# Kernel optimization log

Measured on AMD Instinct MI355X. Metric: run time of the kernel, lower is better.

The kernel has to match this reference:

```python
import jax, jax.numpy as jnp
import numpy as np

N = 16      # manifold_dim
H = 128     # hidden_dim
B = 256     # batch
EPS = 1e-6


def setup_inputs() -> dict:
    key = jax.random.key(0)
    ks = jax.random.split(key, 14)
    def w(k, shape):
        fan_in = shape[0]
        return jax.random.uniform(k, shape, jnp.float32, -1.0, 1.0) / np.sqrt(fan_in)
    return {
        "points": jax.random.normal(ks[0], (B, N), jnp.float32),
        # metric network: N -> H -> N*N
        "mW1": w(ks[1], (N, H)), "mb1": jnp.zeros((H,), jnp.float32),
        "mW2": w(ks[2], (H, N * N)), "mb2": jnp.zeros((N * N,), jnp.float32),
        # christoffel network: 3 -> H -> 1
        "cW1": w(ks[3], (3, H)), "cb1": jnp.zeros((H,), jnp.float32),
        "cW2": w(ks[4], (H, 1)), "cb2": jnp.zeros((1,), jnp.float32),
        # ricci network: 4N -> 2H -> N*N
        "rW1": w(ks[5], (4 * N, 2 * H)), "rb1": jnp.zeros((2 * H,), jnp.float32),
        "rW2": w(ks[6], (2 * H, N * N)), "rb2": jnp.zeros((N * N,), jnp.float32),
    }


def reference(points, mW1, mb1, mW2, mb2, cW1, cb1, cW2, cb2, rW1, rb1, rW2, rb2):
    b = points.shape[0]
    n = N
    # ---- metric: (b, n, n) ----
    mh = jax.nn.relu(points @ mW1 + mb1)
    metric = (mh @ mW2 + mb2).reshape(b, n, n)
    metric = metric + EPS * jnp.eye(n, dtype=metric.dtype)
    metric = 0.5 * (metric + jnp.swapaxes(metric, -2, -1))

    # ---- christoffel: vectorized over all (i,j,k) triples ----
    # inputs per triple: [metric_ij, metric_jk, metric_ki]
    m_ij = jnp.broadcast_to(metric[:, :, :, None], (b, n, n, n))
    m_jk = jnp.broadcast_to(metric[:, None, :, :], (b, n, n, n))
    mT = jnp.swapaxes(metric, -2, -1)  # mT[b,i,k] = metric[b,k,i]
    m_ki = jnp.broadcast_to(mT[:, :, None, :], (b, n, n, n))
    ch_in = jnp.stack([m_ij, m_jk, m_ki], axis=-1)        # (b,n,n,n,3)
    ch_h = jnp.tanh(ch_in @ cW1 + cb1)                    # (b,n,n,n,H)
    christoffel = (ch_h @ cW2 + cb2)[..., 0]              # (b,n,n,n)

    # ---- ricci: vectorized over all (i,j) pairs ----
    p_b = jnp.broadcast_to(points[:, None, None, :], (b, n, n, n))
    m_i = jnp.broadcast_to(metric[:, :, None, :], (b, n, n, n))
    m_j = jnp.broadcast_to(metric[:, None, :, :], (b, n, n, n))
    r_in = jnp.concatenate([p_b, m_i, m_j, christoffel], axis=-1)  # (b,n,n,4n)
    r_h = jax.nn.relu(r_in @ rW1 + rb1)                   # (b,n,n,2H)
    r_out = (r_h @ rW2 + rb2).reshape(b, n, n, n, n)      # (b,i,j,n,n)
    r_out = 0.5 * (r_out + jnp.swapaxes(r_out, -1, -2))
    ricci = r_out.sum(axis=(1, 2)) / (n * n)              # (b,n,n)
    return ricci
```

## Files before the change

kernel.cpp:

```cpp
#include <hip/hip_runtime.h>
#include <hip/hip_bf16.h>

#define NDIM 16
#define HDIM 128
#define BATCH 256
#define EPS_D 1e-6f

typedef float v2f __attribute__((ext_vector_type(2)));
static __device__ __forceinline__ v2f v2(float a, float b) {
  v2f r; r.x = a; r.y = b; return r;
}
static __device__ __forceinline__ v2f splat(float a) {
  v2f r; r.x = a; r.y = a; return r;
}

__global__ __launch_bounds__(256) void metric_proj_kernel(
    const float* __restrict__ points,
    const float* __restrict__ mW1, const float* __restrict__ mb1,
    const float* __restrict__ mW2, const float* __restrict__ mb2,
    const float* __restrict__ rW1, const float* __restrict__ rb1,
    float* __restrict__ metric,
    float* __restrict__ A1, float* __restrict__ Mi, float* __restrict__ Mj,
    float* __restrict__ G) {
  int b = blockIdx.x;
  int t = threadIdx.x;
  __shared__ float p[16];
  __shared__ float mh[128];
  __shared__ float raw[256];
  __shared__ float M[256];
  G[b * 256 + t] = 0.f;
  if (t < 16) p[t] = points[b * 16 + t];
  __syncthreads();
  if (t < 128) {
    float acc = mb1[t];
#pragma unroll
    for (int k = 0; k < 16; ++k) acc = fmaf(p[k], mW1[k * 128 + t], acc);
    mh[t] = fmaxf(acc, 0.f);
  }
  __syncthreads();
  {
    float acc = mb2[t];
#pragma unroll 8
    for (int h = 0; h < 128; ++h) acc = fmaf(mh[h], mW2[h * 256 + t], acc);
    raw[t] = acc;
  }
  __syncthreads();
  {
    int i = t >> 4, j = t & 15;
    float v = 0.5f * (raw[i * 16 + j] + raw[j * 16 + i]);
    if (i == j) v += EPS_D;
    M[t] = v;
    metric[b * 256 + t] = v;
  }
  __syncthreads();
  {
    int h = t;
    float wB[16], wC[16];
#pragma unroll
    for (int c = 0; c < 16; ++c) {
      wB[c] = rW1[(16 + c) * 256 + h];
      wC[c] = rW1[(32 + c) * 256 + h];
    }
    float a = rb1[h];
#pragma unroll
    for (int r = 0; r < 16; ++r) a = fmaf(p[r], rW1[r * 256 + h], a);
    A1[b * 256 + h] = a;
#pragma unroll 2
    for (int i = 0; i < 16; ++i) {
      float mi = 0.f, mj = 0.f;
#pragma unroll
      for (int c = 0; c < 16; ++c) {
        float m = M[i * 16 + c];
        mi = fmaf(m, wB[c], mi);
        mj = fmaf(m, wC[c], mj);
      }
      Mi[(b * 16 + i) * 256 + h] = mi;
      Mj[(b * 16 + i) * 256 + h] = mj;
    }
  }
}

__global__ __launch_bounds__(128, 8) void chr_kernel(
    const float* __restrict__ metric,
    const float* __restrict__ cW1, const float* __restrict__ cb1,
    const float* __restrict__ cW2, const float* __restrict__ cb2,
    const float* __restrict__ rW1,
    const float* __restrict__ A1, const float* __restrict__ Mi,
    const float* __restrict__ Mj,
    float* __restrict__ G) {
  int bi = blockIdx.x;
  int b = bi >> 4, i = bi & 15;
  int t = threadIdx.x;
  int w = t >> 6, l = t & 63;
  __shared__ float M[256];
  __shared__ float4 z[128];
  __shared__ float4 w2p[32];
  __shared__ float4 ch4[64];
  float* chf = (float*)ch4;
  M[t] = metric[b * 256 + t];
  M[t + 128] = metric[b * 256 + t + 128];
  {
    const float S = 2.8853900817779268f;
    z[t] = make_float4(S * cW1[t], S * cW1[128 + t], S * cW1[256 + t],
                       S * cb1[t]);
    ((float*)w2p)[t] = cW2[t];
  }
  __syncthreads();

  {
    int jk0 = w * 128 + l, jk1 = jk0 + 64;
    int j0 = jk0 >> 4, k0 = jk0 & 15;
    int j1 = jk1 >> 4, k1 = jk1 & 15;
    v2f x0 = v2(M[i * 16 + j0], M[i * 16 + j1]);
    v2f x1 = v2(M[j0 * 16 + k0], M[j1 * 16 + k1]);
    v2f x2 = v2(M[k0 * 16 + i], M[k1 * 16 + i]);
    v2f acc = splat(cb2[0]);
    for (int hq = 0; hq < 32; ++hq) {
      float4 W2 = w2p[hq];
      float w2u[4] = {W2.x, W2.y, W2.z, W2.w};
#pragma unroll
      for (int u = 0; u < 4; ++u) {
        float4 Q = z[hq * 4 + u];
        v2f pre = __builtin_elementwise_fma(
            x0, splat(Q.x),
            __builtin_elementwise_fma(
                x1, splat(Q.y),
                __builtin_elementwise_fma(x2, splat(Q.z), splat(Q.w))));
        v2f e;
        e.x = __builtin_amdgcn_exp2f(pre.x);
        e.y = __builtin_amdgcn_exp2f(pre.y);
        v2f ep = e + splat(1.f);
        v2f r;
        r.x = __builtin_amdgcn_rcpf(ep.x);
        r.y = __builtin_amdgcn_rcpf(ep.y);
        v2f th = __builtin_elementwise_fma(splat(-2.f), r, splat(1.f));
        acc = __builtin_elementwise_fma(th, splat(w2u[u]), acc);
      }
    }
    chf[jk0] = acc.x;
    chf[jk1] = acc.y;
  }
  __syncthreads();

  {
    int h2 = 2 * t;
    v2f rc2[16];
#pragma unroll
    for (int kk = 0; kk < 16; ++kk) {
      float2 rv = *(const float2*)&rW1[(48 + kk) * 256 + h2];
      rc2[kk] = v2(rv.x, rv.y);
    }
    float2 a1v = *(const float2*)&A1[b * 256 + h2];
    float2 miv = *(const float2*)&Mi[bi * 256 + h2];
    v2f base = v2(a1v.x + miv.x, a1v.y + miv.y);
    v2f hacc = splat(0.f);
    for (int jj = 0; jj < 16; ++jj) {
      float4 c0 = ch4[jj * 4 + 0];
      float4 c1 = ch4[jj * 4 + 1];
      float4 c2v = ch4[jj * 4 + 2];
      float4 c3 = ch4[jj * 4 + 3];
      float2 mjv = *(const float2*)&Mj[(b * 16 + jj) * 256 + h2];
      v2f cp = base + v2(mjv.x, mjv.y);
      float cc[16] = {c0.x, c0.y, c0.z, c0.w, c1.x, c1.y, c1.z, c1.w,
                      c2v.x, c2v.y, c2v.z, c2v.w, c3.x, c3.y, c3.z, c3.w};
#pragma unroll
      for (int kk = 0; kk < 16; ++kk)
        cp = __builtin_elementwise_fma(splat(cc[kk]), rc2[kk], cp);
      v2f rl;
      rl.x = fmaxf(cp.x, 0.f);
      rl.y = fmaxf(cp.y, 0.f);
      hacc += rl;
    }
    atomicAdd(&G[b * 256 + h2], hacc.x);
    atomicAdd(&G[b * 256 + h2 + 1], hacc.y);
  }
}

__global__ __launch_bounds__(256) void final_kernel(
    const float* __restrict__ G,
    const float* __restrict__ rW2, const float* __restrict__ rb2,
    float* __restrict__ out) {
  int b = blockIdx.x;
  int t = threadIdx.x;
  __shared__ float4 Gs[64];
  __shared__ float T[256];
  if (t < 64) Gs[t] = ((const float4*)(G + b * 256))[t];
  __syncthreads();
  float acc = 256.f * rb2[t];
#pragma unroll 4
  for (int h4 = 0; h4 < 64; ++h4) {
    float4 gg = Gs[h4];
    acc = fmaf(gg.x, rW2[(h4 * 4 + 0) * 256 + t], acc);
    acc = fmaf(gg.y, rW2[(h4 * 4 + 1) * 256 + t], acc);
    acc = fmaf(gg.z, rW2[(h4 * 4 + 2) * 256 + t], acc);
    acc = fmaf(gg.w, rW2[(h4 * 4 + 3) * 256 + t], acc);
  }
  T[t] = acc * (1.f / 256.f);
  __syncthreads();
  int k = t >> 4, lcol = t & 15;
  out[b * 256 + t] = 0.5f * (T[k * 16 + lcol] + T[lcol * 16 + k]);
}

extern "C" void kernel_launch(void* const* d_in, const int* in_sizes, int n_in,
                              void* d_out, int out_size, void* d_ws, size_t ws_size,
                              hipStream_t stream) {
  const float* points = (const float*)d_in[0];
  const float* mW1 = (const float*)d_in[1];
  const float* mb1 = (const float*)d_in[2];
  const float* mW2 = (const float*)d_in[3];
  const float* mb2 = (const float*)d_in[4];
  const float* cW1 = (const float*)d_in[5];
  const float* cb1 = (const float*)d_in[6];
  const float* cW2 = (const float*)d_in[7];
  const float* cb2 = (const float*)d_in[8];
  const float* rW1 = (const float*)d_in[9];
  const float* rb1 = (const float*)d_in[10];
  const float* rW2 = (const float*)d_in[11];
  const float* rb2 = (const float*)d_in[12];
  float* out = (float*)d_out;

  float* ws = (float*)d_ws;
  float* metric = ws;
  float* A1 = metric + 65536;
  float* Mi = A1 + 65536;
  float* Mj = Mi + 1048576;
  float* G = Mj + 1048576;

  metric_proj_kernel<<<BATCH, 256, 0, stream>>>(points, mW1, mb1, mW2, mb2,
                                                rW1, rb1, metric, A1, Mi, Mj, G);
  chr_kernel<<<BATCH * NDIM, 128, 0, stream>>>(metric, cW1, cb1, cW2, cb2, rW1,
                                               A1, Mi, Mj, G);
  final_kernel<<<BATCH, 256, 0, stream>>>(G, rW2, rb2, out);
}
```

Measured before the change: 134.0 us.

## Process two i-rows per chr_kernel block to reuse loaded weights and halve atomics

Each chr_kernel block now handles two i values instead of one: each wave computes the Christoffel values for a full i row (four outputs per lane), and the ricci stage reuses the rW1 register tile and the Mj loads for both rows. This halves the grid, the per-block setup (loading M, z and w2p), the rW1 and Mj reloads, and the atomicAdds into G. In exchange it raises register pressure (launch bounds relaxed from 8 to 4 blocks per CU) and cuts the number of blocks, which could lower occupancy and latency hiding.

```diff
diff --git a/kernel.cpp b/kernel.cpp
--- a/kernel.cpp
+++ b/kernel.cpp
@@ -80,7 +80,7 @@
   }
 }
 
-__global__ __launch_bounds__(128, 8) void chr_kernel(
+__global__ __launch_bounds__(128, 4) void chr_kernel(
     const float* __restrict__ metric,
     const float* __restrict__ cW1, const float* __restrict__ cb1,
     const float* __restrict__ cW2, const float* __restrict__ cb2,
@@ -88,15 +88,15 @@
     const float* __restrict__ A1, const float* __restrict__ Mi,
     const float* __restrict__ Mj,
     float* __restrict__ G) {
-  int bi = blockIdx.x;
-  int b = bi >> 4, i = bi & 15;
+  int blk = blockIdx.x;
+  int b = blk >> 3, ip = blk & 7;
   int t = threadIdx.x;
   int w = t >> 6, l = t & 63;
+  int i = ip * 2 + w;
   __shared__ float M[256];
   __shared__ float4 z[128];
   __shared__ float4 w2p[32];
-  __shared__ float4 ch4[64];
-  float* chf = (float*)ch4;
+  __shared__ float4 ch4[2][64];
   M[t] = metric[b * 256 + t];
   M[t + 128] = metric[b * 256 + t + 128];
   {
@@ -108,42 +108,63 @@
   __syncthreads();
 
   {
-    int jk0 = w * 128 + l, jk1 = jk0 + 64;
-    int j0 = jk0 >> 4, k0 = jk0 & 15;
-    int j1 = jk1 >> 4, k1 = jk1 & 15;
-    v2f x0 = v2(M[i * 16 + j0], M[i * 16 + j1]);
-    v2f x1 = v2(M[j0 * 16 + k0], M[j1 * 16 + k1]);
-    v2f x2 = v2(M[k0 * 16 + i], M[k1 * 16 + i]);
-    v2f acc = splat(cb2[0]);
+    float* chf = (float*)ch4[w];
+    int jA0 = l >> 4, kA0 = l & 15;
+    int jA1 = (l + 64) >> 4, kA1 = (l + 64) & 15;
+    int jB0 = (l + 128) >> 4, kB0 = (l + 128) & 15;
+    int jB1 = (l + 192) >> 4, kB1 = (l + 192) & 15;
+    v2f x0A = v2(M[i * 16 + jA0], M[i * 16 + jA1]);
+    v2f x1A = v2(M[jA0 * 16 + kA0], M[jA1 * 16 + kA1]);
+    v2f x2A = v2(M[kA0 * 16 + i], M[kA1 * 16 + i]);
+    v2f x0B = v2(M[i * 16 + jB0], M[i * 16 + jB1]);
+    v2f x1B = v2(M[jB0 * 16 + kB0], M[jB1 * 16 + kB1]);
+    v2f x2B = v2(M[kB0 * 16 + i], M[kB1 * 16 + i]);
+    v2f accA = splat(cb2[0]);
+    v2f accB = splat(cb2[0]);
     for (int hq = 0; hq < 32; ++hq) {
       float4 W2 = w2p[hq];
       float w2u[4] = {W2.x, W2.y, W2.z, W2.w};
 #pragma unroll
       for (int u = 0; u < 4; ++u) {
         float4 Q = z[hq * 4 + u];
-        v2f pre = __builtin_elementwise_fma(
-            x0, splat(Q.x),
+        v2f preA = __builtin_elementwise_fma(
+            x0A, splat(Q.x),
             __builtin_elementwise_fma(
-                x1, splat(Q.y),
-                __builtin_elementwise_fma(x2, splat(Q.z), splat(Q.w))));
-        v2f e;
-        e.x = __builtin_amdgcn_exp2f(pre.x);
-        e.y = __builtin_amdgcn_exp2f(pre.y);
-        v2f ep = e + splat(1.f);
-        v2f r;
-        r.x = __builtin_amdgcn_rcpf(ep.x);
-        r.y = __builtin_amdgcn_rcpf(ep.y);
-        v2f th = __builtin_elementwise_fma(splat(-2.f), r, splat(1.f));
-        acc = __builtin_elementwise_fma(th, splat(w2u[u]), acc);
+                x1A, splat(Q.y),
+                __builtin_elementwise_fma(x2A, splat(Q.z), splat(Q.w))));
+        v2f preB = __builtin_elementwise_fma(
+            x0B, splat(Q.x),
+            __builtin_elementwise_fma(
+                x1B, splat(Q.y),
+                __builtin_elementwise_fma(x2B, splat(Q.z), splat(Q.w))));
+        v2f eA, eB;
+        eA.x = __builtin_amdgcn_exp2f(preA.x);
+        eA.y = __builtin_amdgcn_exp2f(preA.y);
+        eB.x = __builtin_amdgcn_exp2f(preB.x);
+        eB.y = __builtin_amdgcn_exp2f(preB.y);
+        v2f epA = eA + splat(1.f);
+        v2f epB = eB + splat(1.f);
+        v2f rA, rB;
+        rA.x = __builtin_amdgcn_rcpf(epA.x);
+        rA.y = __builtin_amdgcn_rcpf(epA.y);
+        rB.x = __builtin_amdgcn_rcpf(epB.x);
+        rB.y = __builtin_amdgcn_rcpf(epB.y);
+        v2f thA = __builtin_elementwise_fma(splat(-2.f), rA, splat(1.f));
+        v2f thB = __builtin_elementwise_fma(splat(-2.f), rB, splat(1.f));
+        accA = __builtin_elementwise_fma(thA, splat(w2u[u]), accA);
+        accB = __builtin_elementwise_fma(thB, splat(w2u[u]), accB);
       }
     }
-    chf[jk0] = acc.x;
-    chf[jk1] = acc.y;
+    chf[l] = accA.x;
+    chf[l + 64] = accA.y;
+    chf[l + 128] = accB.x;
+    chf[l + 192] = accB.y;
   }
   __syncthreads();
 
   {
     int h2 = 2 * t;
+    int bi0 = b * 16 + ip * 2, bi1 = bi0 + 1;
     v2f rc2[16];
 #pragma unroll
     for (int kk = 0; kk < 16; ++kk) {
@@ -151,28 +172,44 @@
       rc2[kk] = v2(rv.x, rv.y);
     }
     float2 a1v = *(const float2*)&A1[b * 256 + h2];
-    float2 miv = *(const float2*)&Mi[bi * 256 + h2];
-    v2f base = v2(a1v.x + miv.x, a1v.y + miv.y);
-    v2f hacc = splat(0.f);
+    float2 mi0 = *(const float2*)&Mi[bi0 * 256 + h2];
+    float2 mi1 = *(const float2*)&Mi[bi1 * 256 + h2];
+    v2f base0 = v2(a1v.x + mi0.x, a1v.y + mi0.y);
+    v2f base1 = v2(a1v.x + mi1.x, a1v.y + mi1.y);
+    v2f hacc0 = splat(0.f);
+    v2f hacc1 = splat(0.f);
     for (int jj = 0; jj < 16; ++jj) {
-      float4 c0 = ch4[jj * 4 + 0];
-      float4 c1 = ch4[jj * 4 + 1];
-      float4 c2v = ch4[jj * 4 + 2];
-      float4 c3 = ch4[jj * 4 + 3];
       float2 mjv = *(const float2*)&Mj[(b * 16 + jj) * 256 + h2];
-      v2f cp = base + v2(mjv.x, mjv.y);
-      float cc[16] = {c0.x, c0.y, c0.z, c0.w, c1.x, c1.y, c1.z, c1.w,
-                      c2v.x, c2v.y, c2v.z, c2v.w, c3.x, c3.y, c3.z, c3.w};
-#pragma unroll
-      for (int kk = 0; kk < 16; ++kk)
-        cp = __builtin_elementwise_fma(splat(cc[kk]), rc2[kk], cp);
-      v2f rl;
-      rl.x = fmaxf(cp.x, 0.f);
-      rl.y = fmaxf(cp.y, 0.f);
-      hacc += rl;
-    }
-    atomicAdd(&G[b * 256 + h2], hacc.x);
-    atomicAdd(&G[b * 256 + h2 + 1], hacc.y);
+      v2f mj2 = v2(mjv.x, mjv.y);
+      float4 c0 = ch4[0][jj * 4 + 0];
+      float4 c1 = ch4[0][jj * 4 + 1];
+      float4 c2v = ch4[0][jj * 4 + 2];
+      float4 c3 = ch4[0][jj * 4 + 3];
+      float4 d0 = ch4[1][jj * 4 + 0];
+      float4 d1 = ch4[1][jj * 4 + 1];
+      float4 d2v = ch4[1][jj * 4 + 2];
+      float4 d3 = ch4[1][jj * 4 + 3];
+      v2f cp0 = base0 + mj2;
+      v2f cp1 = base1 + mj2;
+      float cc0[16] = {c0.x, c0.y, c0.z, c0.w, c1.x, c1.y, c1.z, c1.w,
+                       c2v.x, c2v.y, c2v.z, c2v.w, c3.x, c3.y, c3.z, c3.w};
+      float cc1[16] = {d0.x, d0.y, d0.z, d0.w, d1.x, d1.y, d1.z, d1.w,
+                       d2v.x, d2v.y, d2v.z, d2v.w, d3.x, d3.y, d3.z, d3.w};
+#pragma unroll
+      for (int kk = 0; kk < 16; ++kk) {
+        cp0 = __builtin_elementwise_fma(splat(cc0[kk]), rc2[kk], cp0);
+        cp1 = __builtin_elementwise_fma(splat(cc1[kk]), rc2[kk], cp1);
+      }
+      v2f rl0, rl1;
+      rl0.x = fmaxf(cp0.x, 0.f);
+      rl0.y = fmaxf(cp0.y, 0.f);
+      rl1.x = fmaxf(cp1.x, 0.f);
+      rl1.y = fmaxf(cp1.y, 0.f);
+      hacc0 += rl0;
+      hacc1 += rl1;
+    }
+    atomicAdd(&G[b * 256 + h2], hacc0.x + hacc1.x);
+    atomicAdd(&G[b * 256 + h2 + 1], hacc0.y + hacc1.y);
   }
 }
 
@@ -228,7 +265,7 @@
 
   metric_proj_kernel<<<BATCH, 256, 0, stream>>>(points, mW1, mb1, mW2, mb2,
                                                 rW1, rb1, metric, A1, Mi, Mj, G);
-  chr_kernel<<<BATCH * NDIM, 128, 0, stream>>>(metric, cW1, cb1, cW2, cb2, rW1,
-                                               A1, Mi, Mj, G);
+  chr_kernel<<<BATCH * 8, 128, 0, stream>>>(metric, cW1, cb1, cW2, cb2, rW1,
+                                            A1, Mi, Mj, G);
   final_kernel<<<BATCH, 256, 0, stream>>>(G, rW2, rb2, out);
 }
```

New measurement: 140.7 us. +5.0%, slower.
